# Kernel tuning notes

Hardware: AMD Instinct MI355X
Metric: run time of the kernel (lower is better)

The kernel has to match this reference:

```python
import jax, jax.numpy as jnp
import numpy as np

NUM_ANCHORS = 9


def select_tensor(tensor, inds):
    # tensor: (b, 9*c, h, w) -> rows (b*h*w*9, c), gather at inds (faithful to source layout)
    bs, c9, h, w = tensor.shape
    c = c9 // NUM_ANCHORS
    t = tensor.reshape(bs, NUM_ANCHORS, c, h * w).transpose(0, 3, 1, 2).reshape(-1, c)
    return t[inds]


def bilinear_sample(feat, bidx, ys, xs):
    # feat: (b, c, H, W); bidx/ys/xs: (P,). torchvision-style: 0 outside [-1, H]x[-1, W].
    H, W = feat.shape[2], feat.shape[3]
    invalid = (ys < -1.0) | (ys > H) | (xs < -1.0) | (xs > W)
    y = jnp.clip(ys, 0.0, H - 1)
    x = jnp.clip(xs, 0.0, W - 1)
    y0 = jnp.floor(y).astype(jnp.int32)
    x0 = jnp.floor(x).astype(jnp.int32)
    y1 = jnp.minimum(y0 + 1, H - 1)
    x1 = jnp.minimum(x0 + 1, W - 1)
    ly = (y - y0)[:, None]
    lx = (x - x0)[:, None]
    hy = 1.0 - ly
    hx = 1.0 - lx
    v00 = feat[bidx, :, y0, x0]
    v01 = feat[bidx, :, y0, x1]
    v10 = feat[bidx, :, y1, x0]
    v11 = feat[bidx, :, y1, x1]
    out = hy * hx * v00 + hy * lx * v01 + ly * hx * v10 + ly * lx * v11
    return jnp.where(invalid[:, None], 0.0, out)


def roi_align_3x3(feat, boxes, batch_idx):
    # output_size=(3,3), spatial_scale=1, sampling_ratio=1 (one center sample/bin), aligned=False
    OUT = 3
    n = boxes.shape[0]
    x1, y1, x2, y2 = boxes[:, 0], boxes[:, 1], boxes[:, 2], boxes[:, 3]
    roi_w = jnp.maximum(x2 - x1, 1.0)
    roi_h = jnp.maximum(y2 - y1, 1.0)
    bw = roi_w / OUT
    bh = roi_h / OUT
    g = jnp.arange(OUT, dtype=jnp.float32) + 0.5
    ys = jnp.broadcast_to(y1[:, None, None] + g[None, :, None] * bh[:, None, None], (n, OUT, OUT)).reshape(-1)
    xs = jnp.broadcast_to(x1[:, None, None] + g[None, None, :] * bw[:, None, None], (n, OUT, OUT)).reshape(-1)
    bidx = jnp.repeat(batch_idx, OUT * OUT)
    vals = bilinear_sample(feat, bidx, ys, xs)  # (n*9, c)
    return vals.reshape(n, OUT, OUT, feat.shape[1]).transpose(0, 3, 1, 2)  # (n, c, 3, 3)


def setup_inputs() -> dict:
    key = jax.random.key(0)
    ks = jax.random.split(key, 8)
    b, c, h, w = 8, 256, 128, 128
    return {
        "feat": jax.random.normal(ks[0], (b, c, h, w), dtype=jnp.float32),
        "hm": jax.random.uniform(ks[1], (b, 9, h, w), dtype=jnp.float32),
        "wh": jax.random.normal(ks[2], (b, 36, h, w), dtype=jnp.float32) * 4.0,
        "offset": jax.random.normal(ks[3], (b, 18, h, w), dtype=jnp.float32),
        "w_fc1": jax.random.normal(ks[4], (c * 9, 1024), dtype=jnp.float32) * 0.02,
        "b_fc1": jnp.zeros((1024,), dtype=jnp.float32),
        "w_cls": jax.random.normal(ks[5], (1024, 10), dtype=jnp.float32) * 0.02,
        "b_cls": jnp.zeros((10,), dtype=jnp.float32),
        "w_wh": jax.random.normal(ks[6], (1024, 4), dtype=jnp.float32) * 0.02,
        "b_wh": jnp.zeros((4,), dtype=jnp.float32),
        "k": 100,
    }


def reference(feat, hm, wh, offset, w_fc1, b_fc1, w_cls, b_cls, w_wh, b_wh, k):
    bs, _, h, w_ = hm.shape
    hw = h * w_
    # get_inds (inds=None path): topk over (b, h*w*9) with (h, w, anchor) flat layout
    flat = hm.transpose(0, 2, 3, 1).reshape(bs, -1)
    top_v, top_i = jax.lax.top_k(flat, k)
    value = top_v.reshape(-1)
    top_i = top_i.reshape(-1)
    stage1_cls = top_i % NUM_ANCHORS
    pos = (top_i // NUM_ANCHORS) % hw
    inds = pos + jnp.repeat(jnp.arange(bs, dtype=top_i.dtype) * hw, k)
    # select_tensor gathers (stage1 and for_stage2 use the same inds in the inference path)
    wh_sel = select_tensor(wh, inds)       # (b*k, 4)
    off_sel = select_tensor(offset, inds)  # (b*k, 2)
    # box arithmetic (faithful: ys = inds // w keeps the batch offset, as in the source)
    xs = (inds % w_).astype(jnp.float32) + off_sel[:, 0]
    ys = (inds // w_).astype(jnp.float32) + off_sel[:, 1]
    batch_idx = jnp.repeat(jnp.arange(bs), k)
    boxes = jnp.stack([xs + wh_sel[:, 0], ys + wh_sel[:, 1],
                       xs + wh_sel[:, 2], ys + wh_sel[:, 3]], axis=1)
    roi_feat = roi_align_3x3(feat, boxes, batch_idx)  # (b*k, c, 3, 3)
    # stage 2 head
    hdn = jax.nn.relu(roi_feat.reshape(roi_feat.shape[0], -1) @ w_fc1 + b_fc1)
    stage2_cls = hdn @ w_cls + b_cls
    stage2_wh = hdn @ w_wh + b_wh
    return (hm, wh_sel, off_sel, stage1_cls, wh_sel, off_sel, stage2_cls, stage2_wh, inds, value)
```

## Files before the change

kernel.cpp:

```cpp
#include <hip/hip_runtime.h>
#include <hip/hip_bf16.h>
#include <stdint.h>

#define HW      16384
#define W_      128
#define NA      9
#define BS      8
#define K_TOP   100
#define NDET    800
#define MPAD    832
#define C_FEAT  256
#define FC1_IN  2304
#define FC1_OUT 1024

#define O_HM    0
#define O_WH1   1179648
#define O_OFF1  1182848
#define O_S1CLS 1184448
#define O_WH2   1185248
#define O_OFF2  1188448
#define O_CLS   1190048
#define O_SWH   1198048
#define O_INDS  1201248
#define O_VAL   1202048

#define NBIN     4096
#define CAND_MAX 512

typedef __attribute__((ext_vector_type(8))) short short8v;
typedef __attribute__((ext_vector_type(4))) float f32x4;

__device__ __forceinline__ void gload16(const void* g, void* l) {
    __builtin_amdgcn_global_load_lds(
        (const __attribute__((address_space(1))) unsigned int*)g,
        (__attribute__((address_space(3))) unsigned int*)l, 16, 0, 0);
}

__global__ __launch_bounds__(1024) void topk_kernel(const float* __restrict__ hm,
                                                    float* __restrict__ out,
                                                    int* __restrict__ ws_inds) {
    const int b   = blockIdx.x;
    const int tid = threadIdx.x;
    __shared__ unsigned int hist[NBIN];
    __shared__ unsigned long long cand[CAND_MAX];
    __shared__ int s_T;
    __shared__ unsigned int s_cnt;

    for (int i = tid; i < NBIN; i += 1024) hist[i] = 0u;
    if (tid == 0) s_cnt = 0u;
    __syncthreads();

    const float4* hm4 = (const float4*)(hm + (size_t)b * NA * HW);
    for (int i = tid; i < (NA * HW) / 4; i += 1024) {
        float4 v = hm4[i];
        int b0 = max(0, min(NBIN - 1, (int)(v.x * (float)NBIN)));
        int b1 = max(0, min(NBIN - 1, (int)(v.y * (float)NBIN)));
        int b2 = max(0, min(NBIN - 1, (int)(v.z * (float)NBIN)));
        int b3 = max(0, min(NBIN - 1, (int)(v.w * (float)NBIN)));
        atomicAdd(&hist[b0], 1u); atomicAdd(&hist[b1], 1u);
        atomicAdd(&hist[b2], 1u); atomicAdd(&hist[b3], 1u);
    }
    __syncthreads();
    if (tid == 0) {
        unsigned int acc = 0; int T = 0;
        for (int bin = NBIN - 1; bin >= 0; --bin) {
            acc += hist[bin];
            if (acc >= K_TOP) { T = bin; break; }
        }
        s_T = T;
    }
    __syncthreads();
    const int T = s_T;
    for (int i = tid; i < (NA * HW) / 4; i += 1024) {
        float4 v4 = hm4[i];
        float vv[4] = {v4.x, v4.y, v4.z, v4.w};
        #pragma unroll
        for (int e = 0; e < 4; ++e) {
            float v = vv[e];
            int bin = max(0, min(NBIN - 1, (int)(v * (float)NBIN)));
            if (bin >= T) {
                unsigned int p = atomicAdd(&s_cnt, 1u);
                if (p < CAND_MAX) {
                    int idx = i * 4 + e;
                    int a  = idx >> 14;
                    int pp = idx & (HW - 1);
                    unsigned int flat_i = (unsigned int)(pp * NA + a);
                    cand[p] = ((unsigned long long)__float_as_uint(v) << 32)
                            | (unsigned long long)(0xFFFFFFFFu - flat_i);
                }
            }
        }
    }
    __syncthreads();
    unsigned int cnt = s_cnt; if (cnt > CAND_MAX) cnt = CAND_MAX;
    if (tid < CAND_MAX && tid >= (int)cnt) cand[tid] = 0ull;
    __syncthreads();
    for (int k = 2; k <= CAND_MAX; k <<= 1) {
        for (int j = k >> 1; j > 0; j >>= 1) {
            if (tid < CAND_MAX) {
                int i = tid;
                int ixj = i ^ j;
                if (ixj > i) {
                    unsigned long long a = cand[i], bb = cand[ixj];
                    bool up = ((i & k) == 0);
                    if (up ? (a < bb) : (a > bb)) { cand[i] = bb; cand[ixj] = a; }
                }
            }
            __syncthreads();
        }
    }
    if (tid < K_TOP) {
        unsigned long long key = cand[tid];
        float v = __uint_as_float((unsigned int)(key >> 32));
        unsigned int flat_i = 0xFFFFFFFFu - (unsigned int)(key & 0xFFFFFFFFull);
        int a = (int)(flat_i % NA);
        int p = (int)(flat_i / NA);
        int inds = p + b * HW;
        int o = b * K_TOP + tid;
        out[O_VAL + o]   = v;
        out[O_S1CLS + o] = (float)a;
        out[O_INDS + o]  = (float)inds;
        ws_inds[o] = inds;
    }
}

__global__ void gather_kernel(const float* __restrict__ wh,
                              const float* __restrict__ offset,
                              const int* __restrict__ ws_inds,
                              float* __restrict__ out,
                              float* __restrict__ ws_boxes) {
    int n = blockIdx.x * blockDim.x + threadIdx.x;
    if (n >= NDET) return;
    int inds = ws_inds[n];
    int p = inds / NA;
    int a = inds - p * NA;
    float w0 = wh[(size_t)(a * 4 + 0) * HW + p];
    float w1 = wh[(size_t)(a * 4 + 1) * HW + p];
    float w2 = wh[(size_t)(a * 4 + 2) * HW + p];
    float w3 = wh[(size_t)(a * 4 + 3) * HW + p];
    float o0 = offset[(size_t)(a * 2 + 0) * HW + p];
    float o1 = offset[(size_t)(a * 2 + 1) * HW + p];
    out[O_WH1 + n * 4 + 0] = w0; out[O_WH1 + n * 4 + 1] = w1;
    out[O_WH1 + n * 4 + 2] = w2; out[O_WH1 + n * 4 + 3] = w3;
    out[O_WH2 + n * 4 + 0] = w0; out[O_WH2 + n * 4 + 1] = w1;
    out[O_WH2 + n * 4 + 2] = w2; out[O_WH2 + n * 4 + 3] = w3;
    out[O_OFF1 + n * 2 + 0] = o0; out[O_OFF1 + n * 2 + 1] = o1;
    out[O_OFF2 + n * 2 + 0] = o0; out[O_OFF2 + n * 2 + 1] = o1;
    float xs = (float)(inds % W_) + o0;
    float ys = (float)(inds / W_) + o1;
    ws_boxes[n * 4 + 0] = xs + w0;
    ws_boxes[n * 4 + 1] = ys + w1;
    ws_boxes[n * 4 + 2] = xs + w2;
    ws_boxes[n * 4 + 3] = ys + w3;
}

__global__ __launch_bounds__(256) void roi_kernel(const float* __restrict__ feat,
                                                  const float* __restrict__ ws_boxes,
                                                  __hip_bfloat16* __restrict__ ws_roi) {
    int n = blockIdx.x;
    int c = threadIdx.x;
    __hip_bfloat16* op = ws_roi + (size_t)n * FC1_IN + (size_t)c * 9;
    if (n >= NDET) {
        #pragma unroll
        for (int i = 0; i < 9; ++i) op[i] = __float2bfloat16(0.0f);
        return;
    }
    float x1 = ws_boxes[n * 4 + 0], y1 = ws_boxes[n * 4 + 1];
    float x2 = ws_boxes[n * 4 + 2], y2 = ws_boxes[n * 4 + 3];
    int b = n / K_TOP;
    float roi_w = fmaxf(x2 - x1, 1.0f);
    float roi_h = fmaxf(y2 - y1, 1.0f);
    float bw = roi_w / 3.0f;
    float bh = roi_h / 3.0f;
    const float* fb = feat + ((size_t)b * C_FEAT + c) * HW;
    #pragma unroll
    for (int gy = 0; gy < 3; ++gy) {
        float ysf = y1 + ((float)gy + 0.5f) * bh;
        #pragma unroll
        for (int gx = 0; gx < 3; ++gx) {
            float xsf = x1 + ((float)gx + 0.5f) * bw;
            bool invalid = (ysf < -1.0f) || (ysf > 128.0f) || (xsf < -1.0f) || (xsf > 128.0f);
            float y = fminf(fmaxf(ysf, 0.0f), 127.0f);
            float x = fminf(fmaxf(xsf, 0.0f), 127.0f);
            int y0 = (int)floorf(y);
            int x0 = (int)floorf(x);
            int y1i = min(y0 + 1, 127);
            int x1i = min(x0 + 1, 127);
            float ly = y - (float)y0, lx = x - (float)x0;
            float hy = 1.0f - ly, hx = 1.0f - lx;
            float v00 = fb[y0 * W_ + x0],  v01 = fb[y0 * W_ + x1i];
            float v10 = fb[y1i * W_ + x0], v11 = fb[y1i * W_ + x1i];
            float v = hy * hx * v00 + hy * lx * v01 + ly * hx * v10 + ly * lx * v11;
            op[gy * 3 + gx] = __float2bfloat16(invalid ? 0.0f : v);
        }
    }
}

__global__ __launch_bounds__(256) void wt_kernel(const float* __restrict__ w,
                                                 __hip_bfloat16* __restrict__ wt) {
    __shared__ float t[64][65];
    int bk = blockIdx.x * 64;
    int bn = blockIdx.y * 64;
    int tid = threadIdx.x;
    int c = tid & 63, r = tid >> 6;
    for (int k = r; k < 64; k += 4)
        t[k][c] = w[(size_t)(bk + k) * FC1_OUT + bn + c];
    __syncthreads();
    for (int n = r; n < 64; n += 4)
        wt[(size_t)(bn + n) * FC1_IN + bk + c] = __float2bfloat16(t[c][n]);
}

__global__ __launch_bounds__(256) void fc1_mfma(const __hip_bfloat16* __restrict__ A,
                                                const __hip_bfloat16* __restrict__ WT,
                                                const float* __restrict__ bias,
                                                float* __restrict__ C) {
    __shared__ char smem[16384];
    const int tid = threadIdx.x;
    const int w = tid >> 6, l = tid & 63;
    const int bm0 = blockIdx.x * 64, bn0 = blockIdx.y * 64;
    const char* Ab = (const char*)A;
    const char* Bb = (const char*)WT;

    f32x4 acc[2][2];
    #pragma unroll
    for (int i = 0; i < 2; ++i)
        #pragma unroll
        for (int j = 0; j < 2; ++j) acc[i][j] = (f32x4){0.f, 0.f, 0.f, 0.f};

    const int wr = (w >> 1) * 32, wc = (w & 1) * 32;
    const int lrow = l & 15;
    const int lkb  = (l >> 4) * 16;

    for (int k0 = 0; k0 < FC1_IN; k0 += 64) {
        #pragma unroll
        for (int j = 0; j < 4; ++j) {
            int o = j * 4096 + tid * 16;
            const char* src;
            if (o < 8192) {
                int r = o >> 7, bby = o & 127;
                src = Ab + ((size_t)(bm0 + r) * FC1_IN + k0) * 2 + (bby ^ ((r & 7) << 4));
            } else {
                int o2 = o - 8192;
                int r = o2 >> 7, bby = o2 & 127;
                src = Bb + ((size_t)(bn0 + r) * FC1_IN + k0) * 2 + (bby ^ ((r & 7) << 4));
            }
            gload16(src, smem + o);
        }
        __syncthreads();
        #pragma unroll
        for (int kk = 0; kk < 2; ++kk) {
            short8v af[2], bf[2];
            #pragma unroll
            for (int ms = 0; ms < 2; ++ms) {
                int r = wr + ms * 16 + lrow;
                int bby = kk * 64 + lkb;
                af[ms] = *(const short8v*)(smem + r * 128 + (bby ^ ((r & 7) << 4)));
            }
            #pragma unroll
            for (int ns = 0; ns < 2; ++ns) {
                int r = wc + ns * 16 + lrow;
                int bby = kk * 64 + lkb;
                bf[ns] = *(const short8v*)(smem + 8192 + r * 128 + (bby ^ ((r & 7) << 4)));
            }
            #pragma unroll
            for (int ms = 0; ms < 2; ++ms)
                #pragma unroll
                for (int ns = 0; ns < 2; ++ns)
                    acc[ms][ns] = __builtin_amdgcn_mfma_f32_16x16x32_bf16(
                        af[ms], bf[ns], acc[ms][ns], 0, 0, 0);
        }
        __syncthreads();
    }
    const int col = l & 15, rbase = (l >> 4) * 4;
    #pragma unroll
    for (int ms = 0; ms < 2; ++ms)
        #pragma unroll
        for (int ns = 0; ns < 2; ++ns)
            #pragma unroll
            for (int j = 0; j < 4; ++j) {
                int gm = bm0 + wr + ms * 16 + rbase + j;
                int gn = bn0 + wc + ns * 16 + col;
                if (gm < NDET)
                    C[(size_t)gm * FC1_OUT + gn] = fmaxf(acc[ms][ns][j] + bias[gn], 0.0f);
            }
}

__global__ __launch_bounds__(256) void fc2_kernel(const float* __restrict__ hdn,
                                                  const float* __restrict__ w_cls,
                                                  const float* __restrict__ b_cls,
                                                  const float* __restrict__ w_wh,
                                                  const float* __restrict__ b_wh,
                                                  float* __restrict__ out) {
    int n = blockIdx.x;
    int tid = threadIdx.x;
    int lane = tid & 63, wv = tid >> 6;
    const float* h = hdn + (size_t)n * FC1_OUT;
    for (int j = wv; j < 14; j += 4) {
        float s = 0.0f;
        if (j < 10) {
            for (int k2 = lane; k2 < FC1_OUT; k2 += 64) s += h[k2] * w_cls[k2 * 10 + j];
        } else {
            int jj = j - 10;
            for (int k2 = lane; k2 < FC1_OUT; k2 += 64) s += h[k2] * w_wh[k2 * 4 + jj];
        }
        #pragma unroll
        for (int off = 32; off > 0; off >>= 1) s += __shfl_down(s, off);
        if (lane == 0) {
            if (j < 10) out[O_CLS + n * 10 + j] = s + b_cls[j];
            else        out[O_SWH + n * 4 + (j - 10)] = s + b_wh[j - 10];
        }
    }
}

extern "C" void kernel_launch(void* const* d_in, const int* in_sizes, int n_in,
                              void* d_out, int out_size, void* d_ws, size_t ws_size,
                              hipStream_t stream) {
    const float* feat   = (const float*)d_in[0];
    const float* hm     = (const float*)d_in[1];
    const float* wh     = (const float*)d_in[2];
    const float* offset = (const float*)d_in[3];
    const float* w_fc1  = (const float*)d_in[4];
    const float* b_fc1  = (const float*)d_in[5];
    const float* w_cls  = (const float*)d_in[6];
    const float* b_cls  = (const float*)d_in[7];
    const float* w_wh   = (const float*)d_in[8];
    const float* b_wh   = (const float*)d_in[9];
    float* out = (float*)d_out;

    char* ws = (char*)d_ws;
    int*   ws_inds          = (int*)ws;
    float* ws_boxes         = (float*)(ws + 4096);
    __hip_bfloat16* ws_wt   = (__hip_bfloat16*)(ws + 32768);
    __hip_bfloat16* ws_roi  = (__hip_bfloat16*)(ws + 32768 + 4718592);
    float* ws_hdn           = (float*)(ws + 32768 + 4718592 + 3833856);

    hipMemcpyAsync(out + O_HM, hm, (size_t)BS * NA * HW * sizeof(float),
                   hipMemcpyDeviceToDevice, stream);

    topk_kernel<<<BS, 1024, 0, stream>>>(hm, out, ws_inds);
    gather_kernel<<<(NDET + 255) / 256, 256, 0, stream>>>(wh, offset, ws_inds, out, ws_boxes);
    wt_kernel<<<dim3(FC1_IN / 64, FC1_OUT / 64), 256, 0, stream>>>(w_fc1, ws_wt);
    roi_kernel<<<MPAD, 256, 0, stream>>>(feat, ws_boxes, ws_roi);
    fc1_mfma<<<dim3(MPAD / 64, FC1_OUT / 64), 256, 0, stream>>>(ws_roi, ws_wt, b_fc1, ws_hdn);
    fc2_kernel<<<NDET, 256, 0, stream>>>(ws_hdn, w_cls, b_cls, w_wh, b_wh, out);
}
```

Baseline: 313.5 us.

## Split top-k across many blocks, fuse gather, double-buffer fc1, transpose fc2 weights

The single-block-per-batch top-k is split into a multi-block histogram kernel, which also copies hm to the output and replaces the separate memcpy, plus a threshold kernel, a multi-block candidate collect, and a per-batch sort kernel that also absorbs the gather step. The histogram shrinks to 1024 bins. fc1 gains double-buffered LDS staging so loads overlap the MFMA work. fc2 reads a pre-transposed weight matrix with float4 loads. More kernel launches and a memset are added. The coarser bins may admit more candidates near the threshold, risking overflow of the 512 slots.

```diff
diff --git a/kernel.cpp b/kernel.cpp
--- a/kernel.cpp
+++ b/kernel.cpp
@@ -24,8 +24,9 @@
 #define O_INDS  1201248
 #define O_VAL   1202048
 
-#define NBIN     4096
+#define NBIN     1024
 #define CAND_MAX 512
+#define HBLK     36
 
 typedef __attribute__((ext_vector_type(8))) short short8v;
 typedef __attribute__((ext_vector_type(4))) float f32x4;
@@ -36,81 +37,117 @@
         (__attribute__((address_space(3))) unsigned int*)l, 16, 0, 0);
 }
 
-__global__ __launch_bounds__(1024) void topk_kernel(const float* __restrict__ hm,
-                                                    float* __restrict__ out,
-                                                    int* __restrict__ ws_inds) {
-    const int b   = blockIdx.x;
+__device__ __forceinline__ int binof(float v) {
+    return max(0, min(NBIN - 1, (int)(v * (float)NBIN)));
+}
+
+__global__ __launch_bounds__(256) void hist_kernel(const float* __restrict__ hm,
+                                                   float* __restrict__ out,
+                                                   unsigned int* __restrict__ hist) {
     const int tid = threadIdx.x;
-    __shared__ unsigned int hist[NBIN];
-    __shared__ unsigned long long cand[CAND_MAX];
-    __shared__ int s_T;
-    __shared__ unsigned int s_cnt;
-
-    for (int i = tid; i < NBIN; i += 1024) hist[i] = 0u;
-    if (tid == 0) s_cnt = 0u;
-    __syncthreads();
-
-    const float4* hm4 = (const float4*)(hm + (size_t)b * NA * HW);
-    for (int i = tid; i < (NA * HW) / 4; i += 1024) {
-        float4 v = hm4[i];
-        int b0 = max(0, min(NBIN - 1, (int)(v.x * (float)NBIN)));
-        int b1 = max(0, min(NBIN - 1, (int)(v.y * (float)NBIN)));
-        int b2 = max(0, min(NBIN - 1, (int)(v.z * (float)NBIN)));
-        int b3 = max(0, min(NBIN - 1, (int)(v.w * (float)NBIN)));
-        atomicAdd(&hist[b0], 1u); atomicAdd(&hist[b1], 1u);
-        atomicAdd(&hist[b2], 1u); atomicAdd(&hist[b3], 1u);
-    }
-    __syncthreads();
-    if (tid == 0) {
-        unsigned int acc = 0; int T = 0;
-        for (int bin = NBIN - 1; bin >= 0; --bin) {
-            acc += hist[bin];
-            if (acc >= K_TOP) { T = bin; break; }
-        }
-        s_T = T;
-    }
-    __syncthreads();
-    const int T = s_T;
-    for (int i = tid; i < (NA * HW) / 4; i += 1024) {
-        float4 v4 = hm4[i];
+    const int b = blockIdx.x / HBLK, sub = blockIdx.x % HBLK;
+    __shared__ unsigned int lh[NBIN];
+    for (int i = tid; i < NBIN; i += 256) lh[i] = 0u;
+    __syncthreads();
+    const float4* src = (const float4*)(hm + (size_t)b * NA * HW) + sub * 1024;
+    float4*       dst = (float4*)(out + O_HM + (size_t)b * NA * HW) + sub * 1024;
+    #pragma unroll
+    for (int t = 0; t < 4; ++t) {
+        float4 v = src[t * 256 + tid];
+        dst[t * 256 + tid] = v;
+        atomicAdd(&lh[binof(v.x)], 1u);
+        atomicAdd(&lh[binof(v.y)], 1u);
+        atomicAdd(&lh[binof(v.z)], 1u);
+        atomicAdd(&lh[binof(v.w)], 1u);
+    }
+    __syncthreads();
+    for (int i = tid; i < NBIN; i += 256)
+        if (lh[i]) atomicAdd(&hist[b * NBIN + i], lh[i]);
+}
+
+__global__ __launch_bounds__(512) void thresh_kernel(const unsigned int* __restrict__ hist,
+                                                     int* __restrict__ thr) {
+    const int b = threadIdx.x >> 6, lane = threadIdx.x & 63;
+    const unsigned int* h = hist + b * NBIN;
+    unsigned int s = 0;
+    #pragma unroll
+    for (int i = 0; i < 16; ++i) s += h[lane * 16 + i];
+    unsigned int suf = s;
+    #pragma unroll
+    for (int off = 1; off < 64; off <<= 1) {
+        unsigned int o = __shfl_down(suf, off);
+        if (lane + off < 64) suf += o;
+    }
+    unsigned long long mask = __ballot(suf >= K_TOP);
+    int L = 63 - __clzll(mask);
+    unsigned int below = __shfl(suf, L + 1);
+    if (L == 63) below = 0;
+    if (lane == L) {
+        unsigned int acc = below;
+        int T = 16 * L;
+        for (int i = 15; i >= 0; --i) {
+            acc += h[16 * L + i];
+            if (acc >= K_TOP) { T = 16 * L + i; break; }
+        }
+        thr[b] = T;
+    }
+}
+
+__global__ __launch_bounds__(256) void collect_kernel(const float* __restrict__ hm,
+                                                      const int* __restrict__ thr,
+                                                      unsigned int* __restrict__ cnt,
+                                                      unsigned long long* __restrict__ cand) {
+    const int tid = threadIdx.x;
+    const int b = blockIdx.x / HBLK, sub = blockIdx.x % HBLK;
+    const int T = thr[b];
+    const float4* src = (const float4*)(hm + (size_t)b * NA * HW) + sub * 1024;
+    #pragma unroll
+    for (int t = 0; t < 4; ++t) {
+        int i4 = sub * 1024 + t * 256 + tid;
+        float4 v4 = src[t * 256 + tid];
         float vv[4] = {v4.x, v4.y, v4.z, v4.w};
         #pragma unroll
         for (int e = 0; e < 4; ++e) {
-            float v = vv[e];
-            int bin = max(0, min(NBIN - 1, (int)(v * (float)NBIN)));
-            if (bin >= T) {
-                unsigned int p = atomicAdd(&s_cnt, 1u);
+            if (binof(vv[e]) >= T) {
+                unsigned int p = atomicAdd(&cnt[b], 1u);
                 if (p < CAND_MAX) {
-                    int idx = i * 4 + e;
+                    int idx = i4 * 4 + e;
                     int a  = idx >> 14;
                     int pp = idx & (HW - 1);
                     unsigned int flat_i = (unsigned int)(pp * NA + a);
-                    cand[p] = ((unsigned long long)__float_as_uint(v) << 32)
-                            | (unsigned long long)(0xFFFFFFFFu - flat_i);
+                    cand[b * CAND_MAX + p] =
+                        ((unsigned long long)__float_as_uint(vv[e]) << 32)
+                        | (unsigned long long)(0xFFFFFFFFu - flat_i);
                 }
             }
         }
     }
-    __syncthreads();
-    unsigned int cnt = s_cnt; if (cnt > CAND_MAX) cnt = CAND_MAX;
-    if (tid < CAND_MAX && tid >= (int)cnt) cand[tid] = 0ull;
+}
+
+__global__ __launch_bounds__(512) void sort_kernel(const unsigned long long* __restrict__ cand,
+                                                   const unsigned int* __restrict__ cntg,
+                                                   const float* __restrict__ wh,
+                                                   const float* __restrict__ offset,
+                                                   float* __restrict__ out,
+                                                   float* __restrict__ ws_boxes) {
+    const int b = blockIdx.x, tid = threadIdx.x;
+    __shared__ unsigned long long cd[CAND_MAX];
+    unsigned int cnt = cntg[b]; if (cnt > CAND_MAX) cnt = CAND_MAX;
+    cd[tid] = (tid < (int)cnt) ? cand[b * CAND_MAX + tid] : 0ull;
     __syncthreads();
     for (int k = 2; k <= CAND_MAX; k <<= 1) {
         for (int j = k >> 1; j > 0; j >>= 1) {
-            if (tid < CAND_MAX) {
-                int i = tid;
-                int ixj = i ^ j;
-                if (ixj > i) {
-                    unsigned long long a = cand[i], bb = cand[ixj];
-                    bool up = ((i & k) == 0);
-                    if (up ? (a < bb) : (a > bb)) { cand[i] = bb; cand[ixj] = a; }
-                }
+            int i = tid, ixj = i ^ j;
+            if (ixj > i) {
+                unsigned long long a = cd[i], bb = cd[ixj];
+                bool up = ((i & k) == 0);
+                if (up ? (a < bb) : (a > bb)) { cd[i] = bb; cd[ixj] = a; }
             }
             __syncthreads();
         }
     }
     if (tid < K_TOP) {
-        unsigned long long key = cand[tid];
+        unsigned long long key = cd[tid];
         float v = __uint_as_float((unsigned int)(key >> 32));
         unsigned int flat_i = 0xFFFFFFFFu - (unsigned int)(key & 0xFFFFFFFFull);
         int a = (int)(flat_i % NA);
@@ -120,38 +157,27 @@
         out[O_VAL + o]   = v;
         out[O_S1CLS + o] = (float)a;
         out[O_INDS + o]  = (float)inds;
-        ws_inds[o] = inds;
-    }
-}
-
-__global__ void gather_kernel(const float* __restrict__ wh,
-                              const float* __restrict__ offset,
-                              const int* __restrict__ ws_inds,
-                              float* __restrict__ out,
-                              float* __restrict__ ws_boxes) {
-    int n = blockIdx.x * blockDim.x + threadIdx.x;
-    if (n >= NDET) return;
-    int inds = ws_inds[n];
-    int p = inds / NA;
-    int a = inds - p * NA;
-    float w0 = wh[(size_t)(a * 4 + 0) * HW + p];
-    float w1 = wh[(size_t)(a * 4 + 1) * HW + p];
-    float w2 = wh[(size_t)(a * 4 + 2) * HW + p];
-    float w3 = wh[(size_t)(a * 4 + 3) * HW + p];
-    float o0 = offset[(size_t)(a * 2 + 0) * HW + p];
-    float o1 = offset[(size_t)(a * 2 + 1) * HW + p];
-    out[O_WH1 + n * 4 + 0] = w0; out[O_WH1 + n * 4 + 1] = w1;
-    out[O_WH1 + n * 4 + 2] = w2; out[O_WH1 + n * 4 + 3] = w3;
-    out[O_WH2 + n * 4 + 0] = w0; out[O_WH2 + n * 4 + 1] = w1;
-    out[O_WH2 + n * 4 + 2] = w2; out[O_WH2 + n * 4 + 3] = w3;
-    out[O_OFF1 + n * 2 + 0] = o0; out[O_OFF1 + n * 2 + 1] = o1;
-    out[O_OFF2 + n * 2 + 0] = o0; out[O_OFF2 + n * 2 + 1] = o1;
-    float xs = (float)(inds % W_) + o0;
-    float ys = (float)(inds / W_) + o1;
-    ws_boxes[n * 4 + 0] = xs + w0;
-    ws_boxes[n * 4 + 1] = ys + w1;
-    ws_boxes[n * 4 + 2] = xs + w2;
-    ws_boxes[n * 4 + 3] = ys + w3;
+        int p2 = inds / NA;
+        int a2 = inds - p2 * NA;
+        float w0 = wh[(size_t)(a2 * 4 + 0) * HW + p2];
+        float w1 = wh[(size_t)(a2 * 4 + 1) * HW + p2];
+        float w2 = wh[(size_t)(a2 * 4 + 2) * HW + p2];
+        float w3 = wh[(size_t)(a2 * 4 + 3) * HW + p2];
+        float o0 = offset[(size_t)(a2 * 2 + 0) * HW + p2];
+        float o1 = offset[(size_t)(a2 * 2 + 1) * HW + p2];
+        out[O_WH1 + o * 4 + 0] = w0; out[O_WH1 + o * 4 + 1] = w1;
+        out[O_WH1 + o * 4 + 2] = w2; out[O_WH1 + o * 4 + 3] = w3;
+        out[O_WH2 + o * 4 + 0] = w0; out[O_WH2 + o * 4 + 1] = w1;
+        out[O_WH2 + o * 4 + 2] = w2; out[O_WH2 + o * 4 + 3] = w3;
+        out[O_OFF1 + o * 2 + 0] = o0; out[O_OFF1 + o * 2 + 1] = o1;
+        out[O_OFF2 + o * 2 + 0] = o0; out[O_OFF2 + o * 2 + 1] = o1;
+        float xs = (float)(inds % W_) + o0;
+        float ys = (float)(inds / W_) + o1;
+        ws_boxes[o * 4 + 0] = xs + w0;
+        ws_boxes[o * 4 + 1] = ys + w1;
+        ws_boxes[o * 4 + 2] = xs + w2;
+        ws_boxes[o * 4 + 3] = ys + w3;
+    }
 }
 
 __global__ __launch_bounds__(256) void roi_kernel(const float* __restrict__ feat,
@@ -168,10 +194,8 @@
     float x1 = ws_boxes[n * 4 + 0], y1 = ws_boxes[n * 4 + 1];
     float x2 = ws_boxes[n * 4 + 2], y2 = ws_boxes[n * 4 + 3];
     int b = n / K_TOP;
-    float roi_w = fmaxf(x2 - x1, 1.0f);
-    float roi_h = fmaxf(y2 - y1, 1.0f);
-    float bw = roi_w / 3.0f;
-    float bh = roi_h / 3.0f;
+    float bw = fmaxf(x2 - x1, 1.0f) / 3.0f;
+    float bh = fmaxf(y2 - y1, 1.0f) / 3.0f;
     const float* fb = feat + ((size_t)b * C_FEAT + c) * HW;
     #pragma unroll
     for (int gy = 0; gy < 3; ++gy) {
@@ -214,7 +238,7 @@
                                                 const __hip_bfloat16* __restrict__ WT,
                                                 const float* __restrict__ bias,
                                                 float* __restrict__ C) {
-    __shared__ char smem[16384];
+    __shared__ char smem[32768];
     const int tid = threadIdx.x;
     const int w = tid >> 6, l = tid & 63;
     const int bm0 = blockIdx.x * 64, bn0 = blockIdx.y * 64;
@@ -231,7 +255,7 @@
     const int lrow = l & 15;
     const int lkb  = (l >> 4) * 16;
 
-    for (int k0 = 0; k0 < FC1_IN; k0 += 64) {
+    auto STAGE = [&](int k0, int buf) {
         #pragma unroll
         for (int j = 0; j < 4; ++j) {
             int o = j * 4096 + tid * 16;
@@ -244,9 +268,17 @@
                 int r = o2 >> 7, bby = o2 & 127;
                 src = Bb + ((size_t)(bn0 + r) * FC1_IN + k0) * 2 + (bby ^ ((r & 7) << 4));
             }
-            gload16(src, smem + o);
-        }
-        __syncthreads();
+            gload16(src, smem + buf * 16384 + o);
+        }
+    };
+
+    STAGE(0, 0);
+    __syncthreads();
+    int cur = 0;
+    #pragma unroll 1
+    for (int t = 0; t < FC1_IN / 64; ++t) {
+        if (t + 1 < FC1_IN / 64) STAGE((t + 1) * 64, cur ^ 1);
+        char* sb = smem + cur * 16384;
         #pragma unroll
         for (int kk = 0; kk < 2; ++kk) {
             short8v af[2], bf[2];
@@ -254,13 +286,13 @@
             for (int ms = 0; ms < 2; ++ms) {
                 int r = wr + ms * 16 + lrow;
                 int bby = kk * 64 + lkb;
-                af[ms] = *(const short8v*)(smem + r * 128 + (bby ^ ((r & 7) << 4)));
+                af[ms] = *(const short8v*)(sb + r * 128 + (bby ^ ((r & 7) << 4)));
             }
             #pragma unroll
             for (int ns = 0; ns < 2; ++ns) {
                 int r = wc + ns * 16 + lrow;
                 int bby = kk * 64 + lkb;
-                bf[ns] = *(const short8v*)(smem + 8192 + r * 128 + (bby ^ ((r & 7) << 4)));
+                bf[ns] = *(const short8v*)(sb + 8192 + r * 128 + (bby ^ ((r & 7) << 4)));
             }
             #pragma unroll
             for (int ms = 0; ms < 2; ++ms)
@@ -270,6 +302,7 @@
                         af[ms], bf[ns], acc[ms][ns], 0, 0, 0);
         }
         __syncthreads();
+        cur ^= 1;
     }
     const int col = l & 15, rbase = (l >> 4) * 4;
     #pragma unroll
@@ -285,23 +318,29 @@
             }
 }
 
+__global__ __launch_bounds__(256) void fc2prep_kernel(const float* __restrict__ w_cls,
+                                                      const float* __restrict__ w_wh,
+                                                      float* __restrict__ wT14) {
+    int idx = blockIdx.x * 256 + threadIdx.x;
+    int j = idx >> 10, k = idx & 1023;
+    wT14[idx] = (j < 10) ? w_cls[k * 10 + j] : w_wh[k * 4 + (j - 10)];
+}
+
 __global__ __launch_bounds__(256) void fc2_kernel(const float* __restrict__ hdn,
-                                                  const float* __restrict__ w_cls,
+                                                  const float* __restrict__ wT14,
                                                   const float* __restrict__ b_cls,
-                                                  const float* __restrict__ w_wh,
                                                   const float* __restrict__ b_wh,
                                                   float* __restrict__ out) {
     int n = blockIdx.x;
-    int tid = threadIdx.x;
-    int lane = tid & 63, wv = tid >> 6;
-    const float* h = hdn + (size_t)n * FC1_OUT;
+    int lane = threadIdx.x & 63, wv = threadIdx.x >> 6;
+    const float4* h4 = (const float4*)(hdn + (size_t)n * FC1_OUT);
     for (int j = wv; j < 14; j += 4) {
+        const float4* w4 = (const float4*)(wT14 + (size_t)j * FC1_OUT);
         float s = 0.0f;
-        if (j < 10) {
-            for (int k2 = lane; k2 < FC1_OUT; k2 += 64) s += h[k2] * w_cls[k2 * 10 + j];
-        } else {
-            int jj = j - 10;
-            for (int k2 = lane; k2 < FC1_OUT; k2 += 64) s += h[k2] * w_wh[k2 * 4 + jj];
+        #pragma unroll
+        for (int t = 0; t < 4; ++t) {
+            float4 a = h4[t * 64 + lane], b = w4[t * 64 + lane];
+            s += a.x * b.x + a.y * b.y + a.z * b.z + a.w * b.w;
         }
         #pragma unroll
         for (int off = 32; off > 0; off >>= 1) s += __shfl_down(s, off);
@@ -328,19 +367,25 @@
     float* out = (float*)d_out;
 
     char* ws = (char*)d_ws;
-    int*   ws_inds          = (int*)ws;
-    float* ws_boxes         = (float*)(ws + 4096);
-    __hip_bfloat16* ws_wt   = (__hip_bfloat16*)(ws + 32768);
-    __hip_bfloat16* ws_roi  = (__hip_bfloat16*)(ws + 32768 + 4718592);
-    float* ws_hdn           = (float*)(ws + 32768 + 4718592 + 3833856);
-
-    hipMemcpyAsync(out + O_HM, hm, (size_t)BS * NA * HW * sizeof(float),
-                   hipMemcpyDeviceToDevice, stream);
-
-    topk_kernel<<<BS, 1024, 0, stream>>>(hm, out, ws_inds);
-    gather_kernel<<<(NDET + 255) / 256, 256, 0, stream>>>(wh, offset, ws_inds, out, ws_boxes);
-    wt_kernel<<<dim3(FC1_IN / 64, FC1_OUT / 64), 256, 0, stream>>>(w_fc1, ws_wt);
-    roi_kernel<<<MPAD, 256, 0, stream>>>(feat, ws_boxes, ws_roi);
-    fc1_mfma<<<dim3(MPAD / 64, FC1_OUT / 64), 256, 0, stream>>>(ws_roi, ws_wt, b_fc1, ws_hdn);
-    fc2_kernel<<<NDET, 256, 0, stream>>>(ws_hdn, w_cls, b_cls, w_wh, b_wh, out);
-}
+    float*              ws_boxes = (float*)(ws + 4096);
+    unsigned int*       ws_hist  = (unsigned int*)(ws + 20480);
+    unsigned int*       ws_cnt   = (unsigned int*)(ws + 53248);
+    int*                ws_thr   = (int*)(ws + 53280);
+    unsigned long long* ws_cand  = (unsigned long long*)(ws + 57344);
+    __hip_bfloat16*     ws_wt    = (__hip_bfloat16*)(ws + 98304);
+    __hip_bfloat16*     ws_roi   = (__hip_bfloat16*)(ws + 98304 + 4718592);
+    float*              ws_hdn   = (float*)(ws + 98304 + 4718592 + 3833856);
+    float*              ws_wT14  = (float*)(ws + 98304 + 4718592 + 3833856 + 3276800);
+
+    hipMemsetAsync(ws + 20480, 0, 32832, stream);
+
+    hist_kernel   <<<BS * HBLK, 256, 0, stream>>>(hm, out, ws_hist);
+    thresh_kernel <<<1, 512, 0, stream>>>(ws_hist, ws_thr);
+    collect_kernel<<<BS * HBLK, 256, 0, stream>>>(hm, ws_thr, ws_cnt, ws_cand);
+    sort_kernel   <<<BS, 512, 0, stream>>>(ws_cand, ws_cnt, wh, offset, out, ws_boxes);
+    wt_kernel     <<<dim3(FC1_IN / 64, FC1_OUT / 64), 256, 0, stream>>>(w_fc1, ws_wt);
+    roi_kernel    <<<MPAD, 256, 0, stream>>>(feat, ws_boxes, ws_roi);
+    fc1_mfma      <<<dim3(MPAD / 64, FC1_OUT / 64), 256, 0, stream>>>(ws_roi, ws_wt, b_fc1, ws_hdn);
+    fc2prep_kernel<<<56, 256, 0, stream>>>(w_cls, w_wh, ws_wT14);
+    fc2_kernel    <<<NDET, 256, 0, stream>>>(ws_hdn, ws_wT14, b_cls, b_wh, out);
+}
```

After: 288.8 us. 1.09x faster.
